# Optimization experiments

Hardware: AMD Instinct MI355X
Metric: run time of the kernel (lower is better)

The kernel has to match this reference:

```python
import jax, jax.numpy as jnp
import numpy as np

EPS = 1e-5


def reference(hidden_states, mu_x, W_x1, W_x2, x_bias, W_r, W_k, W_v, W_g,
              A_w, B_w, b_w, bonus, gn_weight, gn_bias, W_o):
    B, T, D = hidden_states.shape
    Hh = bonus.shape[0]
    x = hidden_states
    # token shift: delta = shifted(x) - x, shifted pads one zero row at t=0
    shifted = jnp.pad(x, ((0, 0), (1, 0), (0, 0)))[:, :T]
    delta = shifted - x
    # x_proj: LerpLinear(D -> 5*lr) -> tanh -> einsum with second weight viewed [D,5,lr]
    lr = W_x1.shape[0] // 5
    z = jnp.tanh((x + delta * mu_x) @ W_x1.T).reshape(B, T, 5, lr)
    mus = jnp.einsum('blnr,dnr->blnd', z, W_x2.reshape(D, 5, lr)) + x_bias  # [B,T,5,D]
    r_mu, w_mu, k_mu, v_mu, g_mu = (mus[:, :, i] for i in range(5))
    # DDLerpLinear projections: linear(x + delta * mu)
    r = (x + delta * r_mu) @ W_r.T                                 # [B,T,KD]
    w = jnp.tanh((x + delta * w_mu) @ A_w.T) @ B_w.T + b_w          # LoRA w/ tanh
    k = (x + delta * k_mu) @ W_k.T
    v = (x + delta * v_mu) @ W_v.T                                 # [B,T,VD]
    g = (x + delta * g_mu) @ W_g.T
    K = W_r.shape[0] // Hh
    V = W_v.shape[0] // Hh
    r = r.reshape(B, T, Hh, K)
    k = k.reshape(B, T, Hh, K)
    w = -jnp.exp(w.reshape(B, T, Hh, K))  # log-decay, in (-inf, 0)
    v = v.reshape(B, T, Hh, V)
    u = bonus                              # [Hh, K]

    def step(S, inp):
        q_t, k_t, v_t, w_t = inp           # [B,Hh,K],[B,Hh,K],[B,Hh,V],[B,Hh,K]
        kv = k_t[..., :, None] * v_t[..., None, :]                  # [B,Hh,K,V]
        o_t = jnp.einsum('bhk,bhkv->bhv', q_t, S + u[None, :, :, None] * kv)
        S = jnp.exp(w_t)[..., None] * S + kv
        return S, o_t

    S0 = jnp.zeros((B, Hh, K, V), dtype=x.dtype)
    xs = (jnp.swapaxes(r, 0, 1), jnp.swapaxes(k, 0, 1),
          jnp.swapaxes(v, 0, 1), jnp.swapaxes(w, 0, 1))
    _, o = jax.lax.scan(step, S0, xs)       # o: [T,B,Hh,V]
    o = jnp.swapaxes(o, 0, 1)               # [B,T,Hh,V]
    # GroupNorm(num_heads, value_dim): normalize each head's V channels per token
    mean = o.mean(-1, keepdims=True)
    var = o.var(-1, keepdims=True)
    o = (o - mean) / jnp.sqrt(var + EPS)
    o = o.reshape(B, T, Hh * V) * gn_weight + gn_bias
    o = o * jax.nn.silu(g)                  # swish gate
    return o @ W_o.T


def setup_inputs() -> dict:
    key = jax.random.key(0)
    ks = jax.random.split(key, 16)
    B, T, D = 8, 2048, 1024
    Hh, KD, VD, LR, GLR = 4, 512, 1024, 32, 64
    s = 0.02
    w = lambda k, shape: jax.random.normal(k, shape, jnp.float32) * s
    return {
        'hidden_states': jax.random.normal(ks[0], (B, T, D), jnp.float32),
        'mu_x': w(ks[1], (D,)),
        'W_x1': w(ks[2], (5 * LR, D)),
        'W_x2': w(ks[3], (D, 5 * LR)),
        'x_bias': jnp.zeros((5, D), jnp.float32),
        'W_r': w(ks[4], (KD, D)),
        'W_k': w(ks[5], (KD, D)),
        'W_v': w(ks[6], (VD, D)),
        'W_g': w(ks[7], (VD, D)),
        'A_w': w(ks[8], (GLR, D)),
        'B_w': w(ks[9], (KD, GLR)),
        'b_w': jnp.zeros((KD,), jnp.float32),
        'bonus': w(ks[10], (Hh, KD // Hh)),
        'gn_weight': jnp.ones((VD,), jnp.float32),
        'gn_bias': jnp.zeros((VD,), jnp.float32),
        'W_o': w(ks[11], (D, VD)),
    }
```

## Files before the change

### kernel.cpp

```cpp
#include <hip/hip_runtime.h>
#include <hip/hip_bf16.h>
#include <hip/hip_fp16.h>
#include <cstdint>


typedef _Float16 half8 __attribute__((ext_vector_type(8)));
typedef float f32x4 __attribute__((ext_vector_type(4)));

#define CL 256
#define NP (CL / 2)
#define NC 8

__device__ __forceinline__ float hbits2f(unsigned short us) {
    __half h; *reinterpret_cast<unsigned short*>(&h) = us; return __half2float(h);
}
__device__ __forceinline__ unsigned short f2h(float f) {
    __half h = __float2half(f);
    return *reinterpret_cast<unsigned short*>(&h);
}
__device__ __forceinline__ float2 up2(unsigned int u) {
    return make_float2(hbits2f((unsigned short)(u & 0xFFFF)),
                       hbits2f((unsigned short)(u >> 16)));
}
__device__ __forceinline__ void gload_lds16(const void* g, void* l) {
    __builtin_amdgcn_global_load_lds(
        (const __attribute__((address_space(1))) unsigned*)g,
        (__attribute__((address_space(3))) unsigned*)l, 16, 0, 0);
}

__global__ void cast16(const float* __restrict__ src, __half* __restrict__ dst, int n4)
{
    const int i = blockIdx.x * blockDim.x + threadIdx.x;
    if (i >= n4) return;
    const float4 f = *(const float4*)(src + (size_t)i * 4);
    ushort4 u;
    u.x = f2h(f.x); u.y = f2h(f.y); u.z = f2h(f.z); u.w = f2h(f.w);
    *(ushort4*)(dst + (size_t)i * 4) = u;
}

__global__ void k_xw_h(const float* __restrict__ X, const float* __restrict__ mu,
                       __half* __restrict__ XW, int M, int T)
{
    const size_t i4 = (size_t)blockIdx.x * blockDim.x + threadIdx.x;
    if (i4 >= (size_t)M * 256) return;
    const size_t idx = i4 * 4;
    const int m = (int)(idx >> 10);
    const int d = (int)(idx & 1023);
    const int t = m & (T - 1);
    const float4 xv = *(const float4*)(X + idx);
    const float4 m4 = *(const float4*)(mu + d);
    float4 xp = make_float4(0.f, 0.f, 0.f, 0.f);
    if (t > 0) xp = *(const float4*)(X + idx - 1024);
    ushort4 o;
    o.x = f2h(xv.x + (xp.x - xv.x) * m4.x);
    o.y = f2h(xv.y + (xp.y - xv.y) * m4.y);
    o.z = f2h(xv.z + (xp.z - xv.z) * m4.z);
    o.w = f2h(xv.w + (xp.w - xv.w) * m4.w);
    *(ushort4*)(XW + idx) = o;
}

__global__ __launch_bounds__(256) void gemm16(
    const __half* __restrict__ A, int lda,
    const __half* __restrict__ B, int ldb,
    void* __restrict__ Cv, int ldc,
    int M, int N, int K,
    const float* __restrict__ bias, int epi,
    const float* __restrict__ X, int T)
{
    __shared__ __align__(16) _Float16 As[128 * 32];
    __shared__ __align__(16) _Float16 Bs[128 * 32];

    const int tid = threadIdx.x;

    const int nwg = gridDim.x * gridDim.y;
    int p = blockIdx.y * gridDim.x + blockIdx.x;
    if (!(nwg & 7)) p = (p & 7) * (nwg >> 3) + (p >> 3);
    const int bx = p % gridDim.x, by = p / gridDim.x;

    const int m0 = by * 128;
    const int n0 = bx * 128;
    const int wave = tid >> 6, lane = tid & 63;
    const int wm = wave >> 1, wn = wave & 1;
    const int lr = lane & 15, lk = lane >> 4;

    const int srow = tid >> 2;
    const int scol = (tid & 3) * 8;
    const int arow0 = m0 + srow, arow1 = m0 + 64 + srow;
    int brow0 = n0 + srow;      if (brow0 >= N) brow0 = N - 1;
    int brow1 = n0 + 64 + srow; if (brow1 >= N) brow1 = N - 1;
    char* dA = (char*)As + tid * 16;
    char* dB = (char*)Bs + tid * 16;

    f32x4 acc[4][4] = {};

    for (int k0 = 0; k0 < K; k0 += 32) {
        const __half* gA0 = A + (size_t)arow0 * lda + k0 + scol;
        const __half* gA1 = A + (size_t)arow1 * lda + k0 + scol;
        const __half* gB0 = B + (size_t)brow0 * ldb + k0 + scol;
        const __half* gB1 = B + (size_t)brow1 * ldb + k0 + scol;
        __syncthreads();
        gload_lds16(gA0, dA);
        gload_lds16(gA1, dA + 4096);
        gload_lds16(gB0, dB);
        gload_lds16(gB1, dB + 4096);
        __syncthreads();

        half8 af[4], bf[4];
#pragma unroll
        for (int f = 0; f < 4; f++) {
            af[f] = *(const half8*)&As[(wm * 64 + f * 16 + lr) * 32 + lk * 8];
            bf[f] = *(const half8*)&Bs[(wn * 64 + f * 16 + lr) * 32 + lk * 8];
        }
#pragma unroll
        for (int fm = 0; fm < 4; fm++)
#pragma unroll
            for (int fn = 0; fn < 4; fn++)
                acc[fm][fn] = __builtin_amdgcn_mfma_f32_16x16x32_f16(
                    af[fm], bf[fn], acc[fm][fn], 0, 0, 0);
    }

#pragma unroll
    for (int fm = 0; fm < 4; fm++) {
#pragma unroll
        for (int fn = 0; fn < 4; fn++) {
#pragma unroll
            for (int j = 0; j < 4; j++) {
                const int gm = m0 + wm * 64 + fm * 16 + lk * 4 + j;
                const int gn = n0 + wn * 64 + fn * 16 + lr;
                if (gn >= N) continue;
                float a = acc[fm][fn][j];
                if (epi == 1) {
                    a = tanhf(a);
                    ((__half*)Cv)[(size_t)gm * ldc + gn] = __float2half(a);
                } else if (epi == 2) {
                    a += bias[gn];
                    const float xv = X[(size_t)gm * 1024 + gn];
                    float xp = 0.f;
                    if (gm & (T - 1)) xp = X[(size_t)(gm - 1) * 1024 + gn];
                    ((__half*)Cv)[(size_t)gm * ldc + gn] =
                        __float2half(xv + (xp - xv) * a);
                } else if (epi == 3) {
                    a += bias[gn];
                    ((__half*)Cv)[(size_t)gm * ldc + gn] = __float2half(a);
                } else if (epi == 4) {
                    ((float*)Cv)[(size_t)gm * ldc + gn] = a;
                } else {
                    ((__half*)Cv)[(size_t)gm * ldc + gn] = __float2half(a);
                }
            }
        }
    }
}

__global__ __launch_bounds__(256) void k_prep(
    const __half* __restrict__ R, const __half* __restrict__ Kk,
    const __half* __restrict__ W, const float* __restrict__ bonus,
    unsigned* __restrict__ Eu, float* __restrict__ RU, int T)
{
    const int tok = blockIdx.x;
    const int b = tok >> 11, t = tok & 2047;
    const int h = threadIdx.x >> 6, lane = threadIdx.x & 63;
    const size_t base = (size_t)tok * 512 + h * 128 + 2 * lane;
    const unsigned rr = *(const unsigned*)(R + base);
    const unsigned kk = *(const unsigned*)(Kk + base);
    const unsigned ww = *(const unsigned*)(W + base);
    const float2 rf = up2(rr), kf = up2(kk), wf = up2(ww);
    const float d0 = __expf(-__expf(wf.x));
    const float d1 = __expf(-__expf(wf.y));
    const float2 uf = *(const float2*)(bonus + h * 128 + 2 * lane);
    float ru = rf.x * uf.x * kf.x + rf.y * uf.y * kf.y;
#pragma unroll
    for (int off = 1; off < 64; off <<= 1) ru += __shfl_xor(ru, off);
    const int bh = b * 4 + h;
    unsigned* ep = Eu + (size_t)(bh * T + t) * 192;
    uint2 rkw;
    rkw.x = (rr & 0xFFFFu) | (kk << 16);
    rkw.y = (rr >> 16) | (kk & 0xFFFF0000u);
    *(uint2*)(ep + 2 * lane) = rkw;
    ep[128 + lane] = (unsigned)f2h(d0) | ((unsigned)f2h(d1) << 16);
    if (lane == 0) RU[(size_t)bh * T + t] = ru;
}

template<bool PART>
__global__ __launch_bounds__(256) void rwkv_coop(
    const uint4* __restrict__ E, const __half* __restrict__ V,
    const float* __restrict__ RU, const __half* __restrict__ Cin,
    __half* __restrict__ Cout, float* __restrict__ Abuf,
    __half* __restrict__ O, int T)
{
    __shared__ uint4 sE[4][96];
    __shared__ uint4 sV[4][16];
    __shared__ float sRU[4][2];

    const int p = blockIdx.x;
    int bh, c, vq;
    if (PART) {
        const int l = (p & 7) * 112 + (p >> 3);
        bh = l / 28; const int rem = l - bh * 28; c = rem >> 2; vq = rem & 3;
    } else {
        const int l = (p & 7) * 128 + (p >> 3);
        bh = l >> 5; c = (l >> 2) & 7; vq = l & 3;
    }
    const int b = bh >> 2, h = bh & 3;
    const int tid = threadIdx.x;
    const int w = tid >> 6, lane = tid & 63;
    const int kg = tid & 15, vg = tid >> 4;
    const int t0 = c * CL;

    const uint4* Eg = E + (size_t)(bh * T + t0) * 48;
    const uint4* Vgp = (const uint4*)(V + ((size_t)b * T + t0) * 1024 + h * 256 + vq * 64);
    const float* RUp = RU + (size_t)bh * T + t0;
    __half* Op = O + ((size_t)b * T + t0) * 1024 + h * 256 + vq * 64 + vg * 4;

    float S[32];
    float Aacc[8];
    if (!PART && c) {
        const __half* Sp = Cin + ((size_t)(c - 1) * 32 + bh) * 32768 + vq * 64 + vg * 4;
#pragma unroll
        for (int kk = 0; kk < 8; kk++) {
            const ushort4 s4 = *(const ushort4*)(Sp + (size_t)(kg * 8 + kk) * 256);
            S[kk * 4 + 0] = hbits2f(s4.x); S[kk * 4 + 1] = hbits2f(s4.y);
            S[kk * 4 + 2] = hbits2f(s4.z); S[kk * 4 + 3] = hbits2f(s4.w);
        }
    } else {
#pragma unroll
        for (int j = 0; j < 32; j++) S[j] = 0.f;
    }
#pragma unroll
    for (int j = 0; j < 8; j++) Aacc[j] = 1.f;

    const int i0 = (kg * 2) ^ ((kg * 2) >> 3);
    const int i1 = (kg * 2 + 1) ^ ((kg * 2 + 1) >> 3);

#define ISSUE(BE, BV, BR, PP)                                                 \
    if (w < 2 && (PP) < NP) {                                                 \
        const int tt = (PP) * 2 + w;                                          \
        if (lane < 48)      BE = Eg[(size_t)tt * 48 + lane];                  \
        else if (lane < 56) BV = Vgp[(size_t)tt * 128 + (lane - 48)];         \
        if (lane == 56)     BR = RUp[tt];                                     \
    }

#define STAGE(BE, BV, BR, SLOT)                                               \
    if (w < 2) {                                                              \
        if (lane < 32)      sE[SLOT][w * 48 + (lane ^ (lane >> 3))] = BE;     \
        else if (lane < 48) sE[SLOT][w * 48 + lane] = BE;                     \
        else if (lane < 56) sV[SLOT][w * 8 + (lane - 48)] = BV;               \
        if (lane == 56)     sRU[SLOT][w] = BR;                                \
    }

#define BAR() do {                                                            \
        asm volatile("s_waitcnt lgkmcnt(0)" ::: "memory");                    \
        __builtin_amdgcn_s_barrier();                                         \
        __builtin_amdgcn_sched_barrier(0);                                    \
    } while (0)

#define COMPUTE(SLOT, SUB, TT)                                                \
    {                                                                         \
        const uint4 rka = sE[SLOT][(SUB) * 48 + i0];                          \
        const uint4 rkb = sE[SLOT][(SUB) * 48 + i1];                          \
        const uint4 dq  = sE[SLOT][(SUB) * 48 + 32 + kg];                     \
        const uint2 vw  = *(const uint2*)((const unsigned*)&sV[SLOT][(SUB) * 8] + vg * 2); \
        const unsigned rw_[8] = {rka.x, rka.y, rka.z, rka.w,                  \
                                 rkb.x, rkb.y, rkb.z, rkb.w};                 \
        const unsigned dw_[4] = {dq.x, dq.y, dq.z, dq.w};                     \
        float r_[8], k_[8], d_[8], vv_[4];                                    \
        _Pragma("unroll") for (int j = 0; j < 8; j++) {                       \
            const float2 rk = up2(rw_[j]); r_[j] = rk.x; k_[j] = rk.y;        \
        }                                                                     \
        _Pragma("unroll") for (int j = 0; j < 4; j++) {                       \
            const float2 dd = up2(dw_[j]); d_[2 * j] = dd.x; d_[2 * j + 1] = dd.y; \
        }                                                                     \
        { const float2 va = up2(vw.x), vb = up2(vw.y);                        \
          vv_[0] = va.x; vv_[1] = va.y; vv_[2] = vb.x; vv_[3] = vb.y; }       \
        float osum[4] = {0.f, 0.f, 0.f, 0.f};                                 \
        _Pragma("unroll") for (int kk = 0; kk < 8; kk++) {                    \
            _Pragma("unroll") for (int vi = 0; vi < 4; vi++) {                \
                osum[vi] = fmaf(r_[kk], S[kk * 4 + vi], osum[vi]);            \
                S[kk * 4 + vi] = fmaf(d_[kk], S[kk * 4 + vi], k_[kk] * vv_[vi]); \
            }                                                                 \
            if (PART) Aacc[kk] *= d_[kk];                                     \
        }                                                                     \
        if (!PART) {                                                          \
            _Pragma("unroll") for (int vi = 0; vi < 4; vi++) {                \
                osum[vi] += __shfl_xor(osum[vi], 1);                          \
                osum[vi] += __shfl_xor(osum[vi], 2);                          \
                osum[vi] += __shfl_xor(osum[vi], 4);                          \
                osum[vi] += __shfl_xor(osum[vi], 8);                          \
            }                                                                 \
            if (kg == 0) {                                                    \
                const float ru_ = sRU[SLOT][SUB];                             \
                ushort4 ou;                                                   \
                ou.x = f2h(osum[0] + ru_ * vv_[0]);                           \
                ou.y = f2h(osum[1] + ru_ * vv_[1]);                           \
                ou.z = f2h(osum[2] + ru_ * vv_[2]);                           \
                ou.w = f2h(osum[3] + ru_ * vv_[3]);                           \
                *(ushort4*)(Op + (size_t)(TT) * 1024) = ou;                   \
            }                                                                 \
        }                                                                     \
    }

#define COMPUTE2(SLOT, PP)  COMPUTE(SLOT, 0, (PP) * 2) COMPUTE(SLOT, 1, (PP) * 2 + 1)

    uint4 e0 = {}, e1 = {}, e2 = {}, e3 = {};
    uint4 v0 = {}, v1 = {}, v2 = {}, v3 = {};
    float r0 = 0.f, r1 = 0.f, r2 = 0.f, r3 = 0.f;

    ISSUE(e0, v0, r0, 0)
    ISSUE(e1, v1, r1, 1)
    ISSUE(e2, v2, r2, 2)
    ISSUE(e3, v3, r3, 3)
    STAGE(e0, v0, r0, 0)
    BAR();

    for (int ps = 0; ps < NP; ps += 4) {
        STAGE(e1, v1, r1, 1)
        ISSUE(e0, v0, r0, ps + 4)
        COMPUTE2(0, ps)
        BAR();
        STAGE(e2, v2, r2, 2)
        ISSUE(e1, v1, r1, ps + 5)
        COMPUTE2(1, ps + 1)
        BAR();
        STAGE(e3, v3, r3, 3)
        ISSUE(e2, v2, r2, ps + 6)
        COMPUTE2(2, ps + 2)
        BAR();
        if (ps + 4 < NP) STAGE(e0, v0, r0, 0)
        ISSUE(e3, v3, r3, ps + 7)
        COMPUTE2(3, ps + 3)
        BAR();
    }

    if (PART) {
        __half* Cw = Cout + ((size_t)c * 32 + bh) * 32768 + vq * 64 + vg * 4;
#pragma unroll
        for (int kk = 0; kk < 8; kk++) {
            ushort4 s4;
            s4.x = f2h(S[kk * 4 + 0]); s4.y = f2h(S[kk * 4 + 1]);
            s4.z = f2h(S[kk * 4 + 2]); s4.w = f2h(S[kk * 4 + 3]);
            *(ushort4*)(Cw + (size_t)(kg * 8 + kk) * 256) = s4;
        }
        if (vg == 0) {
            float* Aw = Abuf + ((size_t)c * 32 + bh) * 128 + kg * 8;
#pragma unroll
            for (int kk = 0; kk < 8; kk++) Aw[kk] = Aacc[kk];
        }
    }
#undef ISSUE
#undef STAGE
#undef BAR
#undef COMPUTE
#undef COMPUTE2
}

__global__ __launch_bounds__(256) void rwkv_comb(
    __half* __restrict__ C, const float* __restrict__ A)
{
    const int gid = blockIdx.x * 256 + threadIdx.x;
    const int bh = gid >> 15;
    const int elem = gid & 32767;
    const int k = elem >> 8;
    float s = hbits2f(*(const unsigned short*)(C + (size_t)bh * 32768 + elem));
#pragma unroll
    for (int c = 1; c < NC - 1; ++c) {
        const float a = A[(size_t)(c * 32 + bh) * 128 + k];
        __half* cp = C + ((size_t)c * 32 + bh) * 32768 + elem;
        s = a * s + hbits2f(*(const unsigned short*)cp);
        *(unsigned short*)cp = f2h(s);
    }
}

__global__ __launch_bounds__(256) void gn_gate(
    const __half* __restrict__ Obuf, const __half* __restrict__ G,
    const float* __restrict__ gnw, const float* __restrict__ gnb,
    __half* __restrict__ Y)
{
    const int token = blockIdx.x;
    const int wave = threadIdx.x >> 6, lane = threadIdx.x & 63;
    const size_t base = (size_t)token * 1024 + wave * 256 + lane * 4;
    const ushort4 xu = *(const ushort4*)(Obuf + base);
    const float x0 = hbits2f(xu.x), x1 = hbits2f(xu.y),
                x2 = hbits2f(xu.z), x3 = hbits2f(xu.w);
    float sum = x0 + x1 + x2 + x3;
    float ssq = x0 * x0 + x1 * x1 + x2 * x2 + x3 * x3;
#pragma unroll
    for (int off = 32; off >= 1; off >>= 1) {
        sum += __shfl_xor(sum, off);
        ssq += __shfl_xor(ssq, off);
    }
    const float mean = sum * (1.f / 256.f);
    const float var = ssq * (1.f / 256.f) - mean * mean;
    const float rstd = rsqrtf(var + 1e-5f);
    const int c0 = wave * 256 + lane * 4;
    const float4 w4 = *(const float4*)(gnw + c0);
    const float4 b4 = *(const float4*)(gnb + c0);
    const ushort4 gu = *(const ushort4*)(G + base);
    const float g0 = hbits2f(gu.x), g1 = hbits2f(gu.y),
                g2 = hbits2f(gu.z), g3 = hbits2f(gu.w);
    ushort4 y;
    y.x = f2h(((x0 - mean) * rstd * w4.x + b4.x) * (g0 / (1.f + __expf(-g0))));
    y.y = f2h(((x1 - mean) * rstd * w4.y + b4.y) * (g1 / (1.f + __expf(-g1))));
    y.z = f2h(((x2 - mean) * rstd * w4.z + b4.z) * (g2 / (1.f + __expf(-g2))));
    y.w = f2h(((x3 - mean) * rstd * w4.w + b4.w) * (g3 / (1.f + __expf(-g3))));
    *(ushort4*)(Y + base) = y;
}

extern "C" void kernel_launch(void* const* d_in, const int* in_sizes, int n_in,
                              void* d_out, int out_size, void* d_ws, size_t ws_size,
                              hipStream_t stream)
{
    (void)in_sizes; (void)n_in; (void)out_size; (void)ws_size;
    const float* x      = (const float*)d_in[0];
    const float* mu_x   = (const float*)d_in[1];
    const float* W_x1   = (const float*)d_in[2];
    const float* W_x2   = (const float*)d_in[3];
    const float* x_bias = (const float*)d_in[4];
    const float* W_r    = (const float*)d_in[5];
    const float* W_k    = (const float*)d_in[6];
    const float* W_v    = (const float*)d_in[7];
    const float* W_g    = (const float*)d_in[8];
    const float* A_w    = (const float*)d_in[9];
    const float* B_w    = (const float*)d_in[10];
    const float* b_w    = (const float*)d_in[11];
    const float* bonus  = (const float*)d_in[12];
    const float* gnw    = (const float*)d_in[13];
    const float* gnb    = (const float*)d_in[14];
    const float* W_o    = (const float*)d_in[15];

    const int B = 8, T = 2048, M = B * T;

    __half* xwh  = (__half*)d_out;
    __half* inbh = xwh + (size_t)M * 1024;

    __half* z   = (__half*)d_ws;
    __half* w1  = z   + (size_t)M * 160;
    __half* rs  = w1  + (size_t)M * 64;
    __half* ks  = rs  + (size_t)M * 512;
    __half* wsm = ks  + (size_t)M * 512;
    __half* vs  = wsm + (size_t)M * 512;
    __half* gs  = vs  + (size_t)M * 1024;
    float*  ru  = (float*)(gs + (size_t)M * 1024);
    __half* wgt = (__half*)(ru + (size_t)32 * T);
    __half* oh  = rs;
    __half* yb  = wsm;
    __half* Cbuf = wsm;
    float*  Abuf = (float*)z;

    __half* W_x1h = wgt;
    __half* W_x2h = W_x1h + 163840;
    __half* W_rh  = W_x2h + 163840;
    __half* W_kh  = W_rh + 524288;
    __half* W_vh  = W_kh + 524288;
    __half* W_gh  = W_vh + 1048576;
    __half* A_wh  = W_gh + 1048576;
    __half* B_wh  = A_wh + 65536;
    __half* W_oh  = B_wh + 32768;

    const dim3 blk(256);
    auto cgrid = [](int n) { return dim3((n / 4 + 255) / 256); };
    cast16<<<cgrid(163840), blk, 0, stream>>>(W_x1, W_x1h, 163840 / 4);
    cast16<<<cgrid(163840), blk, 0, stream>>>(W_x2, W_x2h, 163840 / 4);
    cast16<<<cgrid(524288), blk, 0, stream>>>(W_r, W_rh, 524288 / 4);
    cast16<<<cgrid(524288), blk, 0, stream>>>(W_k, W_kh, 524288 / 4);
    cast16<<<cgrid(1048576), blk, 0, stream>>>(W_v, W_vh, 1048576 / 4);
    cast16<<<cgrid(1048576), blk, 0, stream>>>(W_g, W_gh, 1048576 / 4);
    cast16<<<cgrid(65536), blk, 0, stream>>>(A_w, A_wh, 65536 / 4);
    cast16<<<cgrid(32768), blk, 0, stream>>>(B_w, B_wh, 32768 / 4);
    cast16<<<cgrid(1048576), blk, 0, stream>>>(W_o, W_oh, 1048576 / 4);

    k_xw_h<<<(M * 256 + 255) / 256, blk, 0, stream>>>(x, mu_x, xwh, M, T);

    auto ggrid = [&](int N) { return dim3((N + 127) / 128, M / 128); };

    gemm16<<<ggrid(160), blk, 0, stream>>>(xwh, 1024, W_x1h, 1024, z, 160,
                                           M, 160, 1024, nullptr, 1, nullptr, T);

    for (int n = 0; n < 5; ++n) {
        gemm16<<<ggrid(1024), blk, 0, stream>>>(z + n * 32, 160, W_x2h + n * 32, 160,
                                                inbh, 1024, M, 1024, 32,
                                                x_bias + n * 1024, 2, x, T);
        if (n == 1) {
            gemm16<<<ggrid(64), blk, 0, stream>>>(inbh, 1024, A_wh, 1024, w1, 64,
                                                  M, 64, 1024, nullptr, 1, nullptr, T);
            gemm16<<<ggrid(512), blk, 0, stream>>>(w1, 64, B_wh, 64, wsm, 512,
                                                   M, 512, 64, b_w, 3, nullptr, T);
        } else {
            __half* Cp = (n == 0) ? rs : (n == 2) ? ks : (n == 3) ? vs : gs;
            const __half* Wp = (n == 0) ? W_rh : (n == 2) ? W_kh : (n == 3) ? W_vh : W_gh;
            const int N = (n == 0 || n == 2) ? 512 : 1024;
            gemm16<<<ggrid(N), blk, 0, stream>>>(inbh, 1024, Wp, 1024, Cp, N,
                                                 M, N, 1024, nullptr, 0, nullptr, T);
        }
    }

    k_prep<<<dim3(M), blk, 0, stream>>>(rs, ks, wsm, bonus,
                                        (unsigned*)d_out, ru, T);

    rwkv_coop<true><<<dim3(896), blk, 0, stream>>>(
        (const uint4*)d_out, vs, ru, Cbuf, Cbuf, Abuf, oh, T);
    rwkv_comb<<<dim3(4096), blk, 0, stream>>>(Cbuf, Abuf);
    rwkv_coop<false><<<dim3(1024), blk, 0, stream>>>(
        (const uint4*)d_out, vs, ru, Cbuf, Cbuf, Abuf, oh, T);

    gn_gate<<<dim3(M), blk, 0, stream>>>(oh, gs, gnw, gnb, yb);

    gemm16<<<ggrid(1024), blk, 0, stream>>>(yb, 1024, W_oh, 1024, d_out, 1024,
                                            M, 1024, 1024, nullptr, 4, nullptr, T);
}
```

Measured before the change: 1.205 ms.

## Split recurrence V dimension into eight slices per head, doubling scan blocks

The chunked WKV recurrence kernels now split each head's 256 value columns into 8 slices of 32 instead of 4 slices of 64. Each thread holds 16 state floats instead of 32, and both recurrence launches use twice as many blocks. The aim is more parallelism, occupancy and latency hiding on the sequential scan. The cost is that the r/k/decay loads, the LDS staging and the cross-lane reductions are repeated for twice as many blocks, and the global loads and stores become narrower.

```diff
diff --git a/kernel.cpp b/kernel.cpp
--- a/kernel.cpp
+++ b/kernel.cpp
@@ -189,17 +189,17 @@
     __half* __restrict__ O, int T)
 {
     __shared__ uint4 sE[4][96];
-    __shared__ uint4 sV[4][16];
+    __shared__ uint4 sV[4][8];
     __shared__ float sRU[4][2];
 
     const int p = blockIdx.x;
     int bh, c, vq;
     if (PART) {
-        const int l = (p & 7) * 112 + (p >> 3);
-        bh = l / 28; const int rem = l - bh * 28; c = rem >> 2; vq = rem & 3;
+        const int l = (p & 7) * 224 + (p >> 3);
+        bh = l / 56; const int rem = l - bh * 56; c = rem >> 3; vq = rem & 7;
     } else {
-        const int l = (p & 7) * 128 + (p >> 3);
-        bh = l >> 5; c = (l >> 2) & 7; vq = l & 3;
+        const int l = (p & 7) * 256 + (p >> 3);
+        bh = l >> 6; c = (l >> 3) & 7; vq = l & 7;
     }
     const int b = bh >> 2, h = bh & 3;
     const int tid = threadIdx.x;
@@ -208,23 +208,23 @@
     const int t0 = c * CL;
 
     const uint4* Eg = E + (size_t)(bh * T + t0) * 48;
-    const uint4* Vgp = (const uint4*)(V + ((size_t)b * T + t0) * 1024 + h * 256 + vq * 64);
+    const uint4* Vgp = (const uint4*)(V + ((size_t)b * T + t0) * 1024 + h * 256 + vq * 32);
     const float* RUp = RU + (size_t)bh * T + t0;
-    __half* Op = O + ((size_t)b * T + t0) * 1024 + h * 256 + vq * 64 + vg * 4;
-
-    float S[32];
+    __half* Op = O + ((size_t)b * T + t0) * 1024 + h * 256 + vq * 32 + vg * 2;
+
+    float S[16];
     float Aacc[8];
     if (!PART && c) {
-        const __half* Sp = Cin + ((size_t)(c - 1) * 32 + bh) * 32768 + vq * 64 + vg * 4;
+        const __half* Sp = Cin + ((size_t)(c - 1) * 32 + bh) * 32768 + vq * 32 + vg * 2;
 #pragma unroll
         for (int kk = 0; kk < 8; kk++) {
-            const ushort4 s4 = *(const ushort4*)(Sp + (size_t)(kg * 8 + kk) * 256);
-            S[kk * 4 + 0] = hbits2f(s4.x); S[kk * 4 + 1] = hbits2f(s4.y);
-            S[kk * 4 + 2] = hbits2f(s4.z); S[kk * 4 + 3] = hbits2f(s4.w);
+            const unsigned s2 = *(const unsigned*)(Sp + (size_t)(kg * 8 + kk) * 256);
+            const float2 sf = up2(s2);
+            S[kk * 2 + 0] = sf.x; S[kk * 2 + 1] = sf.y;
         }
     } else {
 #pragma unroll
-        for (int j = 0; j < 32; j++) S[j] = 0.f;
+        for (int j = 0; j < 16; j++) S[j] = 0.f;
     }
 #pragma unroll
     for (int j = 0; j < 8; j++) Aacc[j] = 1.f;
@@ -232,20 +232,20 @@
     const int i0 = (kg * 2) ^ ((kg * 2) >> 3);
     const int i1 = (kg * 2 + 1) ^ ((kg * 2 + 1) >> 3);
 
-#define ISSUE(BE, BV, BR, PP)                                                 \
+#define ISSUE(BE, BR, PP)                                                     \
     if (w < 2 && (PP) < NP) {                                                 \
         const int tt = (PP) * 2 + w;                                          \
         if (lane < 48)      BE = Eg[(size_t)tt * 48 + lane];                  \
-        else if (lane < 56) BV = Vgp[(size_t)tt * 128 + (lane - 48)];         \
-        if (lane == 56)     BR = RUp[tt];                                     \
-    }
-
-#define STAGE(BE, BV, BR, SLOT)                                               \
+        else if (lane < 52) BE = Vgp[(size_t)tt * 128 + (lane - 48)];         \
+        if (lane == 52)     BR = RUp[tt];                                     \
+    }
+
+#define STAGE(BE, BR, SLOT)                                                   \
     if (w < 2) {                                                              \
         if (lane < 32)      sE[SLOT][w * 48 + (lane ^ (lane >> 3))] = BE;     \
         else if (lane < 48) sE[SLOT][w * 48 + lane] = BE;                     \
-        else if (lane < 56) sV[SLOT][w * 8 + (lane - 48)] = BV;               \
-        if (lane == 56)     sRU[SLOT][w] = BR;                                \
+        else if (lane < 52) sV[SLOT][w * 4 + (lane - 48)] = BE;               \
+        if (lane == 52)     sRU[SLOT][w] = BR;                                \
     }
 
 #define BAR() do {                                                            \
@@ -259,29 +259,28 @@
         const uint4 rka = sE[SLOT][(SUB) * 48 + i0];                          \
         const uint4 rkb = sE[SLOT][(SUB) * 48 + i1];                          \
         const uint4 dq  = sE[SLOT][(SUB) * 48 + 32 + kg];                     \
-        const uint2 vw  = *(const uint2*)((const unsigned*)&sV[SLOT][(SUB) * 8] + vg * 2); \
+        const unsigned vw = ((const unsigned*)&sV[SLOT][(SUB) * 4])[vg];      \
         const unsigned rw_[8] = {rka.x, rka.y, rka.z, rka.w,                  \
                                  rkb.x, rkb.y, rkb.z, rkb.w};                 \
         const unsigned dw_[4] = {dq.x, dq.y, dq.z, dq.w};                     \
-        float r_[8], k_[8], d_[8], vv_[4];                                    \
+        float r_[8], k_[8], d_[8], vv_[2];                                    \
         _Pragma("unroll") for (int j = 0; j < 8; j++) {                       \
             const float2 rk = up2(rw_[j]); r_[j] = rk.x; k_[j] = rk.y;        \
         }                                                                     \
         _Pragma("unroll") for (int j = 0; j < 4; j++) {                       \
             const float2 dd = up2(dw_[j]); d_[2 * j] = dd.x; d_[2 * j + 1] = dd.y; \
         }                                                                     \
-        { const float2 va = up2(vw.x), vb = up2(vw.y);                        \
-          vv_[0] = va.x; vv_[1] = va.y; vv_[2] = vb.x; vv_[3] = vb.y; }       \
-        float osum[4] = {0.f, 0.f, 0.f, 0.f};                                 \
+        { const float2 va = up2(vw); vv_[0] = va.x; vv_[1] = va.y; }          \
+        float osum[2] = {0.f, 0.f};                                           \
         _Pragma("unroll") for (int kk = 0; kk < 8; kk++) {                    \
-            _Pragma("unroll") for (int vi = 0; vi < 4; vi++) {                \
-                osum[vi] = fmaf(r_[kk], S[kk * 4 + vi], osum[vi]);            \
-                S[kk * 4 + vi] = fmaf(d_[kk], S[kk * 4 + vi], k_[kk] * vv_[vi]); \
+            _Pragma("unroll") for (int vi = 0; vi < 2; vi++) {                \
+                osum[vi] = fmaf(r_[kk], S[kk * 2 + vi], osum[vi]);            \
+                S[kk * 2 + vi] = fmaf(d_[kk], S[kk * 2 + vi], k_[kk] * vv_[vi]); \
             }                                                                 \
             if (PART) Aacc[kk] *= d_[kk];                                     \
         }                                                                     \
         if (!PART) {                                                          \
-            _Pragma("unroll") for (int vi = 0; vi < 4; vi++) {                \
+            _Pragma("unroll") for (int vi = 0; vi < 2; vi++) {                \
                 osum[vi] += __shfl_xor(osum[vi], 1);                          \
                 osum[vi] += __shfl_xor(osum[vi], 2);                          \
                 osum[vi] += __shfl_xor(osum[vi], 4);                          \
@@ -289,12 +288,9 @@
             }                                                                 \
             if (kg == 0) {                                                    \
                 const float ru_ = sRU[SLOT][SUB];                             \
-                ushort4 ou;                                                   \
-                ou.x = f2h(osum[0] + ru_ * vv_[0]);                           \
-                ou.y = f2h(osum[1] + ru_ * vv_[1]);                           \
-                ou.z = f2h(osum[2] + ru_ * vv_[2]);                           \
-                ou.w = f2h(osum[3] + ru_ * vv_[3]);                           \
-                *(ushort4*)(Op + (size_t)(TT) * 1024) = ou;                   \
+                const unsigned ou = (unsigned)f2h(osum[0] + ru_ * vv_[0]) |   \
+                                    ((unsigned)f2h(osum[1] + ru_ * vv_[1]) << 16); \
+                *(unsigned*)(Op + (size_t)(TT) * 1024) = ou;                  \
             }                                                                 \
         }                                                                     \
     }
@@ -302,43 +298,41 @@
 #define COMPUTE2(SLOT, PP)  COMPUTE(SLOT, 0, (PP) * 2) COMPUTE(SLOT, 1, (PP) * 2 + 1)
 
     uint4 e0 = {}, e1 = {}, e2 = {}, e3 = {};
-    uint4 v0 = {}, v1 = {}, v2 = {}, v3 = {};
     float r0 = 0.f, r1 = 0.f, r2 = 0.f, r3 = 0.f;
 
-    ISSUE(e0, v0, r0, 0)
-    ISSUE(e1, v1, r1, 1)
-    ISSUE(e2, v2, r2, 2)
-    ISSUE(e3, v3, r3, 3)
-    STAGE(e0, v0, r0, 0)
+    ISSUE(e0, r0, 0)
+    ISSUE(e1, r1, 1)
+    ISSUE(e2, r2, 2)
+    ISSUE(e3, r3, 3)
+    STAGE(e0, r0, 0)
     BAR();
 
     for (int ps = 0; ps < NP; ps += 4) {
-        STAGE(e1, v1, r1, 1)
-        ISSUE(e0, v0, r0, ps + 4)
+        STAGE(e1, r1, 1)
+        ISSUE(e0, r0, ps + 4)
         COMPUTE2(0, ps)
         BAR();
-        STAGE(e2, v2, r2, 2)
-        ISSUE(e1, v1, r1, ps + 5)
+        STAGE(e2, r2, 2)
+        ISSUE(e1, r1, ps + 5)
         COMPUTE2(1, ps + 1)
         BAR();
-        STAGE(e3, v3, r3, 3)
-        ISSUE(e2, v2, r2, ps + 6)
+        STAGE(e3, r3, 3)
+        ISSUE(e2, r2, ps + 6)
         COMPUTE2(2, ps + 2)
         BAR();
-        if (ps + 4 < NP) STAGE(e0, v0, r0, 0)
-        ISSUE(e3, v3, r3, ps + 7)
+        if (ps + 4 < NP) STAGE(e0, r0, 0)
+        ISSUE(e3, r3, ps + 7)
         COMPUTE2(3, ps + 3)
         BAR();
     }
 
     if (PART) {
-        __half* Cw = Cout + ((size_t)c * 32 + bh) * 32768 + vq * 64 + vg * 4;
+        __half* Cw = Cout + ((size_t)c * 32 + bh) * 32768 + vq * 32 + vg * 2;
 #pragma unroll
         for (int kk = 0; kk < 8; kk++) {
-            ushort4 s4;
-            s4.x = f2h(S[kk * 4 + 0]); s4.y = f2h(S[kk * 4 + 1]);
-            s4.z = f2h(S[kk * 4 + 2]); s4.w = f2h(S[kk * 4 + 3]);
-            *(ushort4*)(Cw + (size_t)(kg * 8 + kk) * 256) = s4;
+            const unsigned s2 = (unsigned)f2h(S[kk * 2 + 0]) |
+                                ((unsigned)f2h(S[kk * 2 + 1]) << 16);
+            *(unsigned*)(Cw + (size_t)(kg * 8 + kk) * 256) = s2;
         }
         if (vg == 0) {
             float* Aw = Abuf + ((size_t)c * 32 + bh) * 128 + kg * 8;
@@ -496,10 +490,10 @@
     k_prep<<<dim3(M), blk, 0, stream>>>(rs, ks, wsm, bonus,
                                         (unsigned*)d_out, ru, T);
 
-    rwkv_coop<true><<<dim3(896), blk, 0, stream>>>(
+    rwkv_coop<true><<<dim3(1792), blk, 0, stream>>>(
         (const uint4*)d_out, vs, ru, Cbuf, Cbuf, Abuf, oh, T);
     rwkv_comb<<<dim3(4096), blk, 0, stream>>>(Cbuf, Abuf);
-    rwkv_coop<false><<<dim3(1024), blk, 0, stream>>>(
+    rwkv_coop<false><<<dim3(2048), blk, 0, stream>>>(
         (const uint4*)d_out, vs, ru, Cbuf, Cbuf, Abuf, oh, T);
 
     gn_gate<<<dim3(M), blk, 0, stream>>>(oh, gs, gnw, gnb, yb);
```

New measurement: 1.336 ms. 10.9% more time.

## Replace second chunked scan pass with MFMA correction GEMM over carried states

Applied to the files above, without the earlier changes.

The chunked WKV recurrence previously ran two scan passes: one to compute chunk-end states, then a second full recurrence seeded with the combined carry-in state. Now a single scan computes local outputs from zero state, records decay-scaled queries (r times cumulative decay) and transposed chunk states. A new MFMA GEMM then adds the carry-in contribution (A_scaled × C_prev) to the outputs. This swaps a second sequential scan for a tensor-core matmul. In exchange it adds an extra fp16 buffer write and read, and does fp16 read-modify-write on the output.

```diff
diff --git a/kernel.cpp b/kernel.cpp
--- a/kernel.cpp
+++ b/kernel.cpp
@@ -181,11 +181,10 @@
     if (lane == 0) RU[(size_t)bh * T + t] = ru;
 }
 
-template<bool PART>
-__global__ __launch_bounds__(256) void rwkv_coop(
+__global__ __launch_bounds__(256) void rwkv_scan(
     const uint4* __restrict__ E, const __half* __restrict__ V,
-    const float* __restrict__ RU, const __half* __restrict__ Cin,
-    __half* __restrict__ Cout, float* __restrict__ Abuf,
+    const float* __restrict__ RU, __half* __restrict__ Cout,
+    float* __restrict__ Abuf, __half* __restrict__ Ab,
     __half* __restrict__ O, int T)
 {
     __shared__ uint4 sE[4][96];
@@ -193,41 +192,27 @@
     __shared__ float sRU[4][2];
 
     const int p = blockIdx.x;
-    int bh, c, vq;
-    if (PART) {
-        const int l = (p & 7) * 112 + (p >> 3);
-        bh = l / 28; const int rem = l - bh * 28; c = rem >> 2; vq = rem & 3;
-    } else {
-        const int l = (p & 7) * 128 + (p >> 3);
-        bh = l >> 5; c = (l >> 2) & 7; vq = l & 3;
-    }
+    const int l = (p & 7) * 128 + (p >> 3);
+    const int bh = l >> 5, c = (l >> 2) & 7, vq = l & 3;
     const int b = bh >> 2, h = bh & 3;
     const int tid = threadIdx.x;
     const int w = tid >> 6, lane = tid & 63;
     const int kg = tid & 15, vg = tid >> 4;
     const int t0 = c * CL;
+    const bool TRACK = (vq == 0) && (c != 0);
 
     const uint4* Eg = E + (size_t)(bh * T + t0) * 48;
     const uint4* Vgp = (const uint4*)(V + ((size_t)b * T + t0) * 1024 + h * 256 + vq * 64);
     const float* RUp = RU + (size_t)bh * T + t0;
     __half* Op = O + ((size_t)b * T + t0) * 1024 + h * 256 + vq * 64 + vg * 4;
+    __half* Ap = Ab + ((size_t)bh * T + t0) * 128 + kg * 8;
 
     float S[32];
-    float Aacc[8];
-    if (!PART && c) {
-        const __half* Sp = Cin + ((size_t)(c - 1) * 32 + bh) * 32768 + vq * 64 + vg * 4;
-#pragma unroll
-        for (int kk = 0; kk < 8; kk++) {
-            const ushort4 s4 = *(const ushort4*)(Sp + (size_t)(kg * 8 + kk) * 256);
-            S[kk * 4 + 0] = hbits2f(s4.x); S[kk * 4 + 1] = hbits2f(s4.y);
-            S[kk * 4 + 2] = hbits2f(s4.z); S[kk * 4 + 3] = hbits2f(s4.w);
-        }
-    } else {
-#pragma unroll
-        for (int j = 0; j < 32; j++) S[j] = 0.f;
-    }
-#pragma unroll
-    for (int j = 0; j < 8; j++) Aacc[j] = 1.f;
+    float Dacc[8];
+#pragma unroll
+    for (int j = 0; j < 32; j++) S[j] = 0.f;
+#pragma unroll
+    for (int j = 0; j < 8; j++) Dacc[j] = 1.f;
 
     const int i0 = (kg * 2) ^ ((kg * 2) >> 3);
     const int i1 = (kg * 2 + 1) ^ ((kg * 2 + 1) >> 3);
@@ -272,30 +257,38 @@
         }                                                                     \
         { const float2 va = up2(vw.x), vb = up2(vw.y);                        \
           vv_[0] = va.x; vv_[1] = va.y; vv_[2] = vb.x; vv_[3] = vb.y; }       \
+        if (TRACK) {                                                          \
+            if (vg == 0) {                                                    \
+                unsigned au[4];                                               \
+                _Pragma("unroll") for (int j = 0; j < 4; j++)                 \
+                    au[j] = (unsigned)f2h(r_[2 * j] * Dacc[2 * j]) |          \
+                            ((unsigned)f2h(r_[2 * j + 1] * Dacc[2 * j + 1]) << 16); \
+                uint4 a4; a4.x = au[0]; a4.y = au[1]; a4.z = au[2]; a4.w = au[3]; \
+                *(uint4*)(Ap + (size_t)(TT) * 128) = a4;                      \
+            }                                                                 \
+            _Pragma("unroll") for (int j = 0; j < 8; j++) Dacc[j] *= d_[j];   \
+        }                                                                     \
         float osum[4] = {0.f, 0.f, 0.f, 0.f};                                 \
         _Pragma("unroll") for (int kk = 0; kk < 8; kk++) {                    \
             _Pragma("unroll") for (int vi = 0; vi < 4; vi++) {                \
                 osum[vi] = fmaf(r_[kk], S[kk * 4 + vi], osum[vi]);            \
                 S[kk * 4 + vi] = fmaf(d_[kk], S[kk * 4 + vi], k_[kk] * vv_[vi]); \
             }                                                                 \
-            if (PART) Aacc[kk] *= d_[kk];                                     \
         }                                                                     \
-        if (!PART) {                                                          \
-            _Pragma("unroll") for (int vi = 0; vi < 4; vi++) {                \
-                osum[vi] += __shfl_xor(osum[vi], 1);                          \
-                osum[vi] += __shfl_xor(osum[vi], 2);                          \
-                osum[vi] += __shfl_xor(osum[vi], 4);                          \
-                osum[vi] += __shfl_xor(osum[vi], 8);                          \
-            }                                                                 \
-            if (kg == 0) {                                                    \
-                const float ru_ = sRU[SLOT][SUB];                             \
-                ushort4 ou;                                                   \
-                ou.x = f2h(osum[0] + ru_ * vv_[0]);                           \
-                ou.y = f2h(osum[1] + ru_ * vv_[1]);                           \
-                ou.z = f2h(osum[2] + ru_ * vv_[2]);                           \
-                ou.w = f2h(osum[3] + ru_ * vv_[3]);                           \
-                *(ushort4*)(Op + (size_t)(TT) * 1024) = ou;                   \
-            }                                                                 \
+        _Pragma("unroll") for (int vi = 0; vi < 4; vi++) {                    \
+            osum[vi] += __shfl_xor(osum[vi], 1);                              \
+            osum[vi] += __shfl_xor(osum[vi], 2);                              \
+            osum[vi] += __shfl_xor(osum[vi], 4);                              \
+            osum[vi] += __shfl_xor(osum[vi], 8);                              \
+        }                                                                     \
+        if (kg == 0) {                                                        \
+            const float ru_ = sRU[SLOT][SUB];                                 \
+            ushort4 ou;                                                       \
+            ou.x = f2h(osum[0] + ru_ * vv_[0]);                               \
+            ou.y = f2h(osum[1] + ru_ * vv_[1]);                               \
+            ou.z = f2h(osum[2] + ru_ * vv_[2]);                               \
+            ou.w = f2h(osum[3] + ru_ * vv_[3]);                               \
+            *(ushort4*)(Op + (size_t)(TT) * 1024) = ou;                       \
         }                                                                     \
     }
 
@@ -331,19 +324,23 @@
         BAR();
     }
 
-    if (PART) {
-        __half* Cw = Cout + ((size_t)c * 32 + bh) * 32768 + vq * 64 + vg * 4;
-#pragma unroll
-        for (int kk = 0; kk < 8; kk++) {
-            ushort4 s4;
-            s4.x = f2h(S[kk * 4 + 0]); s4.y = f2h(S[kk * 4 + 1]);
-            s4.z = f2h(S[kk * 4 + 2]); s4.w = f2h(S[kk * 4 + 3]);
-            *(ushort4*)(Cw + (size_t)(kg * 8 + kk) * 256) = s4;
-        }
-        if (vg == 0) {
+    if (c < NC - 1) {
+        __half* Cw = Cout + ((size_t)c * 32 + bh) * 32768 +
+                     (size_t)(vq * 64 + vg * 4) * 128 + kg * 8;
+#pragma unroll
+        for (int vi = 0; vi < 4; vi++) {
+            unsigned su[4];
+#pragma unroll
+            for (int j = 0; j < 4; j++)
+                su[j] = (unsigned)f2h(S[(2 * j) * 4 + vi]) |
+                        ((unsigned)f2h(S[(2 * j + 1) * 4 + vi]) << 16);
+            uint4 s4; s4.x = su[0]; s4.y = su[1]; s4.z = su[2]; s4.w = su[3];
+            *(uint4*)(Cw + (size_t)vi * 128) = s4;
+        }
+        if (TRACK && vg == 0) {
             float* Aw = Abuf + ((size_t)c * 32 + bh) * 128 + kg * 8;
 #pragma unroll
-            for (int kk = 0; kk < 8; kk++) Aw[kk] = Aacc[kk];
+            for (int j = 0; j < 8; j++) Aw[j] = Dacc[j];
         }
     }
 #undef ISSUE
@@ -359,7 +356,7 @@
     const int gid = blockIdx.x * 256 + threadIdx.x;
     const int bh = gid >> 15;
     const int elem = gid & 32767;
-    const int k = elem >> 8;
+    const int k = elem & 127;
     float s = hbits2f(*(const unsigned short*)(C + (size_t)bh * 32768 + elem));
 #pragma unroll
     for (int c = 1; c < NC - 1; ++c) {
@@ -367,6 +364,76 @@
         __half* cp = C + ((size_t)c * 32 + bh) * 32768 + elem;
         s = a * s + hbits2f(*(const unsigned short*)cp);
         *(unsigned short*)cp = f2h(s);
+    }
+}
+
+__global__ __launch_bounds__(256) void corr_gemm(
+    const __half* __restrict__ Abig, const __half* __restrict__ Cbuf,
+    __half* __restrict__ O, int T)
+{
+    __shared__ __align__(16) _Float16 As[128 * 32];
+    __shared__ __align__(16) _Float16 Bs[128 * 32];
+
+    const int tid = threadIdx.x;
+    const int p = blockIdx.x;
+    const int l = (p & 7) * 112 + (p >> 3);
+    const int bhc = l >> 2, mt = (l >> 1) & 1, nt = l & 1;
+    const int bh = bhc / 7, ci = bhc - bh * 7;
+    const int b = bh >> 2, h = bh & 3;
+    const int t0 = (ci + 1) * CL + mt * 128;
+
+    const __half* Ag = Abig + ((size_t)bh * T + t0) * 128;
+    const __half* Bg = Cbuf + ((size_t)ci * 32 + bh) * 32768 + (size_t)nt * 128 * 128;
+    __half* Og = O + ((size_t)b * T + t0) * 1024 + h * 256 + nt * 128;
+
+    const int wave = tid >> 6, lane = tid & 63;
+    const int wm = wave >> 1, wn = wave & 1;
+    const int lr = lane & 15, lk = lane >> 4;
+    const int srow = tid >> 2;
+    const int scol = (tid & 3) * 8;
+    char* dA = (char*)As + tid * 16;
+    char* dB = (char*)Bs + tid * 16;
+
+    f32x4 acc[4][4] = {};
+
+    for (int k0 = 0; k0 < 128; k0 += 32) {
+        const __half* gA0 = Ag + (size_t)srow * 128 + k0 + scol;
+        const __half* gA1 = Ag + (size_t)(64 + srow) * 128 + k0 + scol;
+        const __half* gB0 = Bg + (size_t)srow * 128 + k0 + scol;
+        const __half* gB1 = Bg + (size_t)(64 + srow) * 128 + k0 + scol;
+        __syncthreads();
+        gload_lds16(gA0, dA);
+        gload_lds16(gA1, dA + 4096);
+        gload_lds16(gB0, dB);
+        gload_lds16(gB1, dB + 4096);
+        __syncthreads();
+
+        half8 af[4], bf[4];
+#pragma unroll
+        for (int f = 0; f < 4; f++) {
+            af[f] = *(const half8*)&As[(wm * 64 + f * 16 + lr) * 32 + lk * 8];
+            bf[f] = *(const half8*)&Bs[(wn * 64 + f * 16 + lr) * 32 + lk * 8];
+        }
+#pragma unroll
+        for (int fm = 0; fm < 4; fm++)
+#pragma unroll
+            for (int fn = 0; fn < 4; fn++)
+                acc[fm][fn] = __builtin_amdgcn_mfma_f32_16x16x32_f16(
+                    af[fm], bf[fn], acc[fm][fn], 0, 0, 0);
+    }
+
+#pragma unroll
+    for (int fm = 0; fm < 4; fm++) {
+#pragma unroll
+        for (int fn = 0; fn < 4; fn++) {
+#pragma unroll
+            for (int j = 0; j < 4; j++) {
+                const int row = wm * 64 + fm * 16 + lk * 4 + j;
+                const int col = wn * 64 + fn * 16 + lr;
+                __half* op = Og + (size_t)row * 1024 + col;
+                *op = __float2half(__half2float(*op) + acc[fm][fn][j]);
+            }
+        }
     }
 }
 
@@ -431,6 +498,7 @@
 
     __half* xwh  = (__half*)d_out;
     __half* inbh = xwh + (size_t)M * 1024;
+    __half* Abig = (__half*)((char*)d_out + (size_t)48 * 1024 * 1024);
 
     __half* z   = (__half*)d_ws;
     __half* w1  = z   + (size_t)M * 160;
@@ -496,11 +564,10 @@
     k_prep<<<dim3(M), blk, 0, stream>>>(rs, ks, wsm, bonus,
                                         (unsigned*)d_out, ru, T);
 
-    rwkv_coop<true><<<dim3(896), blk, 0, stream>>>(
-        (const uint4*)d_out, vs, ru, Cbuf, Cbuf, Abuf, oh, T);
+    rwkv_scan<<<dim3(1024), blk, 0, stream>>>(
+        (const uint4*)d_out, vs, ru, Cbuf, Abuf, Abig, oh, T);
     rwkv_comb<<<dim3(4096), blk, 0, stream>>>(Cbuf, Abuf);
-    rwkv_coop<false><<<dim3(1024), blk, 0, stream>>>(
-        (const uint4*)d_out, vs, ru, Cbuf, Cbuf, Abuf, oh, T);
+    corr_gemm<<<dim3(896), blk, 0, stream>>>(Abig, Cbuf, oh, T);
 
     gn_gate<<<dim3(M), blk, 0, stream>>>(oh, gs, gnw, gnb, yb);
 
```

Measured after the change: 1.155 ms. 4.1% less time.
